# Optimization experiments

Hardware: AMD Instinct MI355X
Metric: run time of the kernel (lower is better)

The kernel has to match this reference:

```python
import jax, jax.numpy as jnp
import numpy as np

B, S, H = 2, 2048, 1024
NH = 16
HD = H // NH  # 64


def _linear_params(key, fan_in, fan_out):
    k1, k2 = jax.random.split(key)
    bound = 1.0 / np.sqrt(fan_in)
    W = jax.random.uniform(k1, (fan_in, fan_out), jnp.float32, -bound, bound)
    b = jax.random.uniform(k2, (fan_out,), jnp.float32, -bound, bound)
    return W, b


def setup_inputs() -> dict:
    key = jax.random.key(0)
    ks = jax.random.split(key, 7)
    hidden_states = jax.random.normal(ks[0], (B, S, H), jnp.float32)
    governance_embeddings = jax.random.normal(ks[1], (B, H), jnp.float32)
    Wq, bq = _linear_params(ks[2], H, H)
    Wk, bk = _linear_params(ks[3], H, H)
    Wv, bv = _linear_params(ks[4], H, H)
    Wgq, bgq = _linear_params(ks[5], H, H)
    Wgk, bgk = _linear_params(ks[6], H, H)
    return {
        'hidden_states': hidden_states,
        'governance_embeddings': governance_embeddings,
        'Wq': Wq, 'bq': bq, 'Wk': Wk, 'bk': bk, 'Wv': Wv, 'bv': bv,
        'Wgq': Wgq, 'bgq': bgq, 'Wgk': Wgk, 'bgk': bgk,
    }


def reference(hidden_states, governance_embeddings, Wq, bq, Wk, bk, Wv, bv, Wgq, bgq, Wgk, bgk):
    b, s, h = hidden_states.shape
    # QKV projections -> [b, nh, s, hd]
    def heads(x):
        return x.reshape(b, s, NH, HD).transpose(0, 2, 1, 3)
    q = heads(hidden_states @ Wq + bq)
    k = heads(hidden_states @ Wk + bk)
    v = heads(hidden_states @ Wv + bv)

    scale = jnp.float32(1.0 / np.sqrt(HD))
    scores = jnp.einsum('bhid,bhjd->bhij', q, k) * scale  # [b,nh,s,s]

    # governance bias: one query per example vs per-token keys (unscaled)
    gq = (governance_embeddings @ Wgq + bgq).reshape(b, NH, HD)      # [b,nh,hd]
    gk = (hidden_states @ Wgk + bgk).reshape(b, s, NH, HD)           # [b,s,nh,hd]
    gov_scores = jnp.einsum('bhd,bshd->bhs', gq, gk)                 # [b,nh,s]

    # bias is constant along key dim (torch expand on last axis)
    combined = scores + 0.1 * gov_scores[..., :, None]

    probs = jax.nn.softmax(combined, axis=-1)  # dropout = identity (eval)
    context = jnp.einsum('bhij,bhjd->bhid', probs, v)
    context = context.transpose(0, 2, 1, 3).reshape(b, s, h)

    entropy = -jnp.sum(probs * jnp.log(probs + 1e-8), axis=-1).mean()
    influence = jnp.abs(gov_scores).mean()  # mean over expanded tensor == mean over [b,nh,s]
    concentration = probs.max(axis=-1).mean()
    return context, entropy, influence, concentration
```

## Files before the change

kernel.cpp:

```cpp
#include <hip/hip_runtime.h>


typedef unsigned short u16;
typedef __attribute__((ext_vector_type(8))) short bf16x8;
typedef __attribute__((ext_vector_type(4))) float f32x4;
typedef __attribute__((ext_vector_type(4))) float float4v;

typedef const __attribute__((address_space(1))) void gvoid_t;
typedef __attribute__((address_space(3))) void lvoid_t;

__device__ __forceinline__ void gl_lds16(const void* g, void* l) {
  __builtin_amdgcn_global_load_lds((gvoid_t*)g, (lvoid_t*)l, 16, 0, 0);
}

__device__ __forceinline__ u16 f2bf(float x) {
  union { float f; unsigned u; } v; v.f = x;
  unsigned r = v.u + 0x7fffu + ((v.u >> 16) & 1u);
  return (u16)(r >> 16);
}
__device__ __forceinline__ float bf2f(u16 h) {
  union { unsigned u; float f; } v; v.u = ((unsigned)h) << 16; return v.f;
}
__device__ __forceinline__ unsigned pk2(float hi, float lo) {
  union { float f; unsigned u; } a, b; a.f = hi; b.f = lo;
  return __builtin_amdgcn_perm(a.u, b.u, 0x07060302u);
}

__global__ void prep(const float* __restrict__ hs,
                     const float* __restrict__ W0, const float* __restrict__ W1,
                     const float* __restrict__ W2, const float* __restrict__ W3,
                     const float* __restrict__ ge, const float* __restrict__ Wgq,
                     u16* __restrict__ hsB, u16* __restrict__ WB,
                     float* __restrict__ gq_part) {
  int bx = blockIdx.x, tid = threadIdx.x;
  if (bx < 2048) {
    int i = bx * 256 + tid;
    const float4v* in4 = (const float4v*)hs;
    float4v a = in4[i * 2], b = in4[i * 2 + 1];
    bf16x8 v;
    v[0] = (short)f2bf(a.x); v[1] = (short)f2bf(a.y);
    v[2] = (short)f2bf(a.z); v[3] = (short)f2bf(a.w);
    v[4] = (short)f2bf(b.x); v[5] = (short)f2bf(b.y);
    v[6] = (short)f2bf(b.z); v[7] = (short)f2bf(b.w);
    *(bf16x8*)&hsB[(size_t)i * 8] = v;
    return;
  }
  if (bx < 2560) {
    int idx = bx - 2048;
    int kb = idx & 127, mat = idx >> 7;
    const float* W = (mat == 0) ? W0 : (mat == 1) ? W1 : (mat == 2) ? W2 : W3;
    int n0 = tid * 4;
    float4v r[8];
#pragma unroll
    for (int j = 0; j < 8; ++j)
      r[j] = *(const float4v*)&W[(size_t)(kb * 8 + j) * 1024 + n0];
#pragma unroll
    for (int c = 0; c < 4; ++c) {
      uint4 o;
      o.x = pk2(r[1][c], r[0][c]); o.y = pk2(r[3][c], r[2][c]);
      o.z = pk2(r[5][c], r[4][c]); o.w = pk2(r[7][c], r[6][c]);
      *(uint4*)&WB[(size_t)(mat * 1024 + n0 + c) * 1024 + kb * 8] = o;
    }
    return;
  }
  {
    int idx = bx - 2560;
    int kb = idx >> 1, b = idx & 1;
    int col0 = tid * 4;
    float4v s = {0.f, 0.f, 0.f, 0.f};
    for (int k = kb * 32; k < kb * 32 + 32; ++k) {
      float g = ge[b * 1024 + k];
      float4v w = *(const float4v*)&Wgq[(size_t)k * 1024 + col0];
      s.x += g * w.x; s.y += g * w.y; s.z += g * w.z; s.w += g * w.w;
    }
    *(float4v*)&gq_part[(size_t)idx * 1024 + col0] = s;
  }
}

__global__ __launch_bounds__(256, 3) void gemm_qkvg(
    const u16* __restrict__ A, const u16* __restrict__ Bw,
    const float* __restrict__ bq, const float* __restrict__ bk,
    const float* __restrict__ bv, const float* __restrict__ bgk,
    const float* __restrict__ bgq, const float* __restrict__ gq_part,
    u16* __restrict__ Qb, u16* __restrict__ Kb,
    u16* __restrict__ GKb, u16* __restrict__ Vt,
    float* __restrict__ gq_final, float* __restrict__ acc3) {
  if (blockIdx.x == 1024) {
    int tid = threadIdx.x;
    if (tid < 3) acc3[tid] = 0.f;
#pragma unroll
    for (int i = 0; i < 8; ++i) {
      int t = tid + i * 256;
      float s = bgq[t & 1023];
      for (int kb = 0; kb < 32; ++kb) s += gq_part[(size_t)(kb * 2 + (t >> 10)) * 1024 + (t & 1023)];
      gq_final[t] = s;
    }
    return;
  }
  __shared__ __align__(16) u16 As[128 * 32];
  __shared__ __align__(16) u16 Bs[128 * 32];
  const int tid = threadIdx.x, lane = tid & 63, wv = tid >> 6;
  const int li = lane & 15, quad = lane >> 4;
  const int bid = blockIdx.x;
  const int nb = bid & 31, mb = bid >> 5;
  const u16* Ap = A + (size_t)(mb * 128) * 1024;
  const u16* Bp = Bw + (size_t)(nb * 128) * 1024;
  const int wm0 = (wv >> 1) * 64, wn0 = (wv & 1) * 64;

  f32x4 acc[4][4];
#pragma unroll
  for (int t = 0; t < 4; ++t)
#pragma unroll
    for (int u = 0; u < 4; ++u) acc[t][u] = (f32x4){0.f, 0.f, 0.f, 0.f};

  for (int kt = 0; kt < 32; ++kt) {
    __syncthreads();
#pragma unroll
    for (int jj = 0; jj < 2; ++jj) {
      int j = wv * 2 + jj;
      int row = j * 16 + (lane >> 2);
      int co = lane & 3;
      gl_lds16(Ap + (size_t)row * 1024 + kt * 32 + co * 8, &As[j * 512]);
      gl_lds16(Bp + (size_t)row * 1024 + kt * 32 + co * 8, &Bs[j * 512]);
    }
    __syncthreads();
    bf16x8 af[4], bf[4];
#pragma unroll
    for (int t = 0; t < 4; ++t)
      af[t] = *(const bf16x8*)&As[(wm0 + t * 16 + li) * 32 + quad * 8];
#pragma unroll
    for (int u = 0; u < 4; ++u)
      bf[u] = *(const bf16x8*)&Bs[(wn0 + u * 16 + li) * 32 + quad * 8];
#pragma unroll
    for (int t = 0; t < 4; ++t)
#pragma unroll
      for (int u = 0; u < 4; ++u)
        acc[t][u] = __builtin_amdgcn_mfma_f32_16x16x32_bf16(af[t], bf[u], acc[t][u], 0, 0, 0);
  }

  const int nbase = nb * 128;
  const int mat = nbase >> 10;
  if (mat == 2) {
#pragma unroll
    for (int t = 0; t < 4; ++t)
#pragma unroll
      for (int u = 0; u < 4; ++u) {
        int col = (nbase & 1023) + wn0 + u * 16 + li;
        float bb = bv[col];
        int row = mb * 128 + wm0 + t * 16 + quad * 4;
        int b = row >> 11, s = row & 2047;
        uint2 w;
        w.x = pk2(acc[t][u][1] + bb, acc[t][u][0] + bb);
        w.y = pk2(acc[t][u][3] + bb, acc[t][u][2] + bb);
        *(uint2*)&Vt[(size_t)b * (1024 * 2048) + (size_t)col * 2048 + s] = w;
      }
  } else {
    const float* bias = (mat == 0) ? bq : (mat == 1) ? bk : bgk;
    u16* outp = (mat == 0) ? Qb : (mat == 1) ? Kb : GKb;
    const float qscale = (mat == 0) ? 0.18033688f : 1.0f;
#pragma unroll
    for (int t = 0; t < 4; ++t)
#pragma unroll
      for (int u = 0; u < 4; ++u) {
        int col = (nbase & 1023) + wn0 + u * 16 + li;
        float bb = bias[col];
#pragma unroll
        for (int r = 0; r < 4; ++r) {
          int row = mb * 128 + wm0 + t * 16 + quad * 4 + r;
          outp[(size_t)row * 1024 + col] = f2bf((acc[t][u][r] + bb) * qscale);
        }
      }
  }
}

__global__ __launch_bounds__(256, 2) void attn_gov(
    const u16* __restrict__ Qb, const u16* __restrict__ Kb,
    const u16* __restrict__ Vt, const u16* __restrict__ GKb,
    const float* __restrict__ gq_final, float* __restrict__ out,
    float* __restrict__ acc3 ) {
  __shared__ __align__(16) u16 Ks[2][128 * 64];
  __shared__ __align__(16) u16 Vs[2][64 * 128];
  __shared__ __align__(16) u16 Ps[4][16 * 36];
  __shared__ float red[8];

  const int tid = threadIdx.x, lane = tid & 63, wv = tid >> 6;
  const int li = lane & 15, quad = lane >> 4;

  if (blockIdx.x >= 512) {
    int wid = (blockIdx.x - 512) * 4 + wv;
    int b = wid >> 11, s = wid & 2047;
    const u16* gk = GKb + (size_t)(b * 2048 + s) * 1024 + lane * 16;
    const float* gqp = gq_final + b * 1024 + lane * 16;
    bf16x8 g0 = *(const bf16x8*)gk, g1 = *(const bf16x8*)(gk + 8);
    float4v q0 = *(const float4v*)&gqp[0], q1 = *(const float4v*)&gqp[4];
    float4v q2 = *(const float4v*)&gqp[8], q3 = *(const float4v*)&gqp[12];
    float sum = 0.f;
    sum += bf2f((u16)g0[0]) * q0.x + bf2f((u16)g0[1]) * q0.y +
           bf2f((u16)g0[2]) * q0.z + bf2f((u16)g0[3]) * q0.w;
    sum += bf2f((u16)g0[4]) * q1.x + bf2f((u16)g0[5]) * q1.y +
           bf2f((u16)g0[6]) * q1.z + bf2f((u16)g0[7]) * q1.w;
    sum += bf2f((u16)g1[0]) * q2.x + bf2f((u16)g1[1]) * q2.y +
           bf2f((u16)g1[2]) * q2.z + bf2f((u16)g1[3]) * q2.w;
    sum += bf2f((u16)g1[4]) * q3.x + bf2f((u16)g1[5]) * q3.y +
           bf2f((u16)g1[6]) * q3.z + bf2f((u16)g1[7]) * q3.w;
    sum += __shfl_xor(sum, 1, 64);
    sum += __shfl_xor(sum, 2, 64);
    float v = ((lane & 3) == 0) ? fabsf(sum) : 0.f;
    v += __shfl_xor(v, 4, 64);  v += __shfl_xor(v, 8, 64);
    v += __shfl_xor(v, 16, 64); v += __shfl_xor(v, 32, 64);
    if (lane == 0) red[wv] = v;
    __syncthreads();
    if (tid == 0) atomicAdd(&acc3[2], red[0] + red[1] + red[2] + red[3]);
    return;
  }

  const int bx = blockIdx.x;
  const int bh = bx & 31, qb = bx >> 5;
  const int b = bh >> 4, h = bh & 15;
  const int wq0 = wv * 32;

  const u16* Qp = Qb + (size_t)(b * 2048 + qb * 128 + wq0) * 1024 + h * 64;
  const u16* Kp = Kb + (size_t)(b * 2048) * 1024 + h * 64;
  const u16* Vp = Vt + (size_t)b * (1024 * 2048) + (size_t)(h * 64) * 2048;

  bf16x8 qf[2][2];
#pragma unroll
  for (int t = 0; t < 2; ++t)
#pragma unroll
    for (int kc = 0; kc < 2; ++kc)
      qf[t][kc] = *(const bf16x8*)&Qp[(size_t)(t * 16 + li) * 1024 + kc * 32 + quad * 8];

  float m_st[2], l_st[2], e_st[2];
  f32x4 accO[4][2];
#pragma unroll
  for (int t = 0; t < 2; ++t) { m_st[t] = -3.0e38f; l_st[t] = 0.f; e_st[t] = 0.f; }
#pragma unroll
  for (int mt = 0; mt < 4; ++mt)
#pragma unroll
    for (int t = 0; t < 2; ++t) accO[mt][t] = (f32x4){0.f, 0.f, 0.f, 0.f};

#pragma unroll
  for (int jj = 0; jj < 4; ++jj) {
    int j = wv * 4 + jj;
    int row = j * 8 + (lane >> 3);
    int c16 = (lane & 7) ^ (row & 7);
    gl_lds16(Kp + (size_t)row * 1024 + c16 * 8, &Ks[0][j * 512]);
  }
#pragma unroll
  for (int jj = 0; jj < 4; ++jj) {
    int j = wv * 4 + jj;
    int row = j * 4 + (lane >> 4);
    int c16 = (lane & 15) ^ (row & 7);
    gl_lds16(Vp + (size_t)row * 2048 + c16 * 8, &Vs[0][j * 512]);
  }

  for (int kt = 0; kt < 16; ++kt) {
    const int cur = kt & 1;
    __syncthreads();
    if (kt < 15) {
      const u16* Kpt = Kp + (size_t)((kt + 1) * 128) * 1024;
#pragma unroll
      for (int jj = 0; jj < 4; ++jj) {
        int j = wv * 4 + jj;
        int row = j * 8 + (lane >> 3);
        int c16 = (lane & 7) ^ (row & 7);
        gl_lds16(Kpt + (size_t)row * 1024 + c16 * 8, &Ks[cur ^ 1][j * 512]);
      }
#pragma unroll
      for (int jj = 0; jj < 4; ++jj) {
        int j = wv * 4 + jj;
        int row = j * 4 + (lane >> 4);
        int c16 = (lane & 15) ^ (row & 7);
        gl_lds16(Vp + (size_t)row * 2048 + (kt + 1) * 128 + c16 * 8, &Vs[cur ^ 1][j * 512]);
      }
    }
    const u16* KsC = &Ks[cur][0];
    const u16* VsC = &Vs[cur][0];

    f32x4 S[8][2];
#pragma unroll
    for (int u = 0; u < 8; ++u) {
      int row = u * 16 + li;
      bf16x8 a0 = *(const bf16x8*)&KsC[row * 64 + ((quad) ^ (li & 7)) * 8];
      bf16x8 a1 = *(const bf16x8*)&KsC[row * 64 + ((4 + quad) ^ (li & 7)) * 8];
#pragma unroll
      for (int t = 0; t < 2; ++t) {
        f32x4 c = {0.f, 0.f, 0.f, 0.f};
        c = __builtin_amdgcn_mfma_f32_16x16x32_bf16(a0, qf[t][0], c, 0, 0, 0);
        c = __builtin_amdgcn_mfma_f32_16x16x32_bf16(a1, qf[t][1], c, 0, 0, 0);
        S[u][t] = c;
      }
    }

#pragma unroll
    for (int t = 0; t < 2; ++t) {
      float cmx = m_st[t], ps = 0.f, es = 0.f;
#pragma unroll
      for (int u = 0; u < 8; ++u)
#pragma unroll
        for (int r = 0; r < 4; ++r) {
          float s = S[u][t][r];
          cmx = fmaxf(cmx, s);
          float p = exp2f(s);
          ps += p;
          es = __builtin_fmaf(p, s, es);
          S[u][t][r] = p;
        }
      m_st[t] = cmx;
      l_st[t] += ps;
      e_st[t] += es;
    }

    u16* Pw = &Ps[wv][0];
#pragma unroll
    for (int c = 0; c < 4; ++c) {
      bf16x8 av[4];
#pragma unroll
      for (int mt = 0; mt < 4; ++mt) {
        int row = mt * 16 + li;
        av[mt] = *(const bf16x8*)&VsC[row * 128 + ((c * 4 + quad) ^ (li & 7)) * 8];
      }
#pragma unroll
      for (int t = 0; t < 2; ++t) {
        uint2 w0, w1;
        w0.x = pk2(S[2 * c][t][1], S[2 * c][t][0]);
        w0.y = pk2(S[2 * c][t][3], S[2 * c][t][2]);
        w1.x = pk2(S[2 * c + 1][t][1], S[2 * c + 1][t][0]);
        w1.y = pk2(S[2 * c + 1][t][3], S[2 * c + 1][t][2]);
        *(uint2*)&Pw[li * 36 + quad * 4] = w0;
        *(uint2*)&Pw[li * 36 + 16 + quad * 4] = w1;
        bf16x8 bp = *(const bf16x8*)&Pw[li * 36 + quad * 8];
#pragma unroll
        for (int mt = 0; mt < 4; ++mt)
          accO[mt][t] = __builtin_amdgcn_mfma_f32_16x16x32_bf16(av[mt], bp, accO[mt][t], 0, 0, 0);
      }
    }
  }

  float* outp = out + (size_t)(b * 2048 + qb * 128 + wq0) * 1024 + h * 64;
  float entw = 0.f, concw = 0.f;
#pragma unroll
  for (int t = 0; t < 2; ++t) {
    float lsum = l_st[t];
    lsum += __shfl_xor(lsum, 16, 64); lsum += __shfl_xor(lsum, 32, 64);
    float esum = e_st[t];
    esum += __shfl_xor(esum, 16, 64); esum += __shfl_xor(esum, 32, 64);
    float mm = m_st[t];
    mm = fmaxf(mm, __shfl_xor(mm, 16, 64)); mm = fmaxf(mm, __shfl_xor(mm, 32, 64));
    float inv = 1.0f / lsum;
    entw += __logf(lsum) - 0.69314718f * esum * inv;
    concw += exp2f(mm) * inv;
#pragma unroll
    for (int mt = 0; mt < 4; ++mt) {
      f32x4 o = accO[mt][t];
      o[0] *= inv; o[1] *= inv; o[2] *= inv; o[3] *= inv;
      *(float4v*)&outp[(size_t)(t * 16 + li) * 1024 + mt * 16 + quad * 4] = *(float4v*)&o;
    }
  }
#pragma unroll
  for (int off = 1; off < 64; off <<= 1) {
    entw += __shfl_xor(entw, off, 64);
    concw += __shfl_xor(concw, off, 64);
  }
  if (lane == 0) { red[wv] = entw * 0.25f; red[4 + wv] = concw * 0.25f; }
  __syncthreads();
  if (tid == 0) {
    atomicAdd(&acc3[0], red[0] + red[1] + red[2] + red[3]);
    atomicAdd(&acc3[1], red[4] + red[5] + red[6] + red[7]);
  }
}

__global__ void finalize(const float* __restrict__ acc3, float* __restrict__ out) {
  if (threadIdx.x == 0) {
    out[0] = acc3[0] * (1.f / 65536.f);
    out[1] = acc3[2] * (1.f / 65536.f);
    out[2] = acc3[1] * (1.f / 65536.f);
  }
}

extern "C" void kernel_launch(void* const* d_in, const int* in_sizes, int n_in,
                              void* d_out, int out_size, void* d_ws, size_t ws_size,
                              hipStream_t stream) {
  (void)in_sizes; (void)n_in; (void)out_size; (void)ws_size;
  const float* hs  = (const float*)d_in[0];
  const float* ge  = (const float*)d_in[1];
  const float* Wq  = (const float*)d_in[2];
  const float* bq  = (const float*)d_in[3];
  const float* Wk  = (const float*)d_in[4];
  const float* bk  = (const float*)d_in[5];
  const float* Wv  = (const float*)d_in[6];
  const float* bv  = (const float*)d_in[7];
  const float* Wgq = (const float*)d_in[8];
  const float* bgq = (const float*)d_in[9];
  const float* Wgk = (const float*)d_in[10];
  const float* bgk = (const float*)d_in[11];

  char* ws = (char*)d_ws;
  u16* hsB = (u16*)(ws);
  u16* WB  = (u16*)(ws + (size_t)(8 << 20));
  u16* Qb  = (u16*)(ws + (size_t)(16 << 20));
  u16* Kb  = (u16*)(ws + (size_t)(24 << 20));
  u16* Vt  = (u16*)(ws + (size_t)(32 << 20));
  u16* GKb = (u16*)(ws + (size_t)(40 << 20));
  float* gq_part  = (float*)(ws + (size_t)(48 << 20));
  float* gq_final = (float*)(ws + (size_t)(48 << 20) + 262144);
  float* acc3     = (float*)(ws + (size_t)(48 << 20) + 524288);
  float* out = (float*)d_out;

  prep<<<2624, 256, 0, stream>>>(hs, Wq, Wk, Wv, Wgk, ge, Wgq, hsB, WB, gq_part);
  gemm_qkvg<<<1025, 256, 0, stream>>>(hsB, WB, bq, bk, bv, bgk, bgq, gq_part,
                                      Qb, Kb, GKb, Vt, gq_final, acc3);
  attn_gov<<<1536, 256, 0, stream>>>(Qb, Kb, Vt, GKb, gq_final, out, acc3);
  finalize<<<1, 64, 0, stream>>>(acc3, out + 4194304);
}
```

Before: 254.9 us.

## Use 32x32 MFMA with permlane P reshuffle in attention; split gov kernel; tiled weight transpose

The attention inner loop moves from 16x16x32 MFMA tiles to 32x32x16 tiles, one query row per lane pair. The P tile is reshaped in registers with permlane32_swap (ds_bpermute as a fallback) instead of a round trip through shared memory. The governance-score reduction becomes its own kernel instead of extra blocks in the attention launch. The weight conversion in prep now goes through a shared-memory tiled transpose with coalesced reads and writes. Together these aim to cut LDS traffic and instruction count in attention and make the weight conversion coalesced, at the cost of an extra launch and higher register pressure from the 16-float accumulators.

```diff
diff --git a/kernel.cpp b/kernel.cpp
--- a/kernel.cpp
+++ b/kernel.cpp
@@ -4,7 +4,10 @@
 typedef unsigned short u16;
 typedef __attribute__((ext_vector_type(8))) short bf16x8;
 typedef __attribute__((ext_vector_type(4))) float f32x4;
+typedef __attribute__((ext_vector_type(16))) float f32x16;
+typedef __attribute__((ext_vector_type(4))) u16 u16x4;
 typedef __attribute__((ext_vector_type(4))) float float4v;
+typedef __attribute__((ext_vector_type(2))) unsigned uint2v;
 
 typedef const __attribute__((address_space(1))) void gvoid_t;
 typedef __attribute__((address_space(3))) void lvoid_t;
@@ -24,6 +27,29 @@
 __device__ __forceinline__ unsigned pk2(float hi, float lo) {
   union { float f; unsigned u; } a, b; a.f = hi; b.f = lo;
   return __builtin_amdgcn_perm(a.u, b.u, 0x07060302u);
+}
+__device__ __forceinline__ bf16x8 mk8(unsigned a, unsigned b, unsigned c, unsigned d) {
+  union { unsigned u[4]; bf16x8 v; } x;
+  x.u[0] = a; x.u[1] = b; x.u[2] = c; x.u[3] = d; return x.v;
+}
+
+#if defined(__has_builtin)
+#if __has_builtin(__builtin_amdgcn_permlane32_swap)
+#define HAVE_PLSWAP 1
+#endif
+#endif
+
+__device__ __forceinline__ void plswap(unsigned& a, unsigned& b, int lane) {
+#ifdef HAVE_PLSWAP
+  uint2v r = __builtin_amdgcn_permlane32_swap(a, b, false, false);
+  a = r.x; b = r.y;
+#else
+  unsigned ca = __builtin_amdgcn_ds_bpermute((lane ^ 32) << 2, a);
+  unsigned cb = __builtin_amdgcn_ds_bpermute((lane ^ 32) << 2, b);
+  unsigned na = (lane < 32) ? a : cb;
+  unsigned nb = (lane < 32) ? ca : b;
+  a = na; b = nb;
+#endif
 }
 
 __global__ void prep(const float* __restrict__ hs,
@@ -32,6 +58,7 @@
                      const float* __restrict__ ge, const float* __restrict__ Wgq,
                      u16* __restrict__ hsB, u16* __restrict__ WB,
                      float* __restrict__ gq_part) {
+  __shared__ __align__(16) u16 T[64][72];
   int bx = blockIdx.x, tid = threadIdx.x;
   if (bx < 2048) {
     int i = bx * 256 + tid;
@@ -45,26 +72,33 @@
     *(bf16x8*)&hsB[(size_t)i * 8] = v;
     return;
   }
-  if (bx < 2560) {
+  if (bx < 3072) {
     int idx = bx - 2048;
-    int kb = idx & 127, mat = idx >> 7;
+    int mat = idx >> 8, sub = idx & 255;
     const float* W = (mat == 0) ? W0 : (mat == 1) ? W1 : (mat == 2) ? W2 : W3;
-    int n0 = tid * 4;
-    float4v r[8];
-#pragma unroll
-    for (int j = 0; j < 8; ++j)
-      r[j] = *(const float4v*)&W[(size_t)(kb * 8 + j) * 1024 + n0];
-#pragma unroll
-    for (int c = 0; c < 4; ++c) {
-      uint4 o;
-      o.x = pk2(r[1][c], r[0][c]); o.y = pk2(r[3][c], r[2][c]);
-      o.z = pk2(r[5][c], r[4][c]); o.w = pk2(r[7][c], r[6][c]);
-      *(uint4*)&WB[(size_t)(mat * 1024 + n0 + c) * 1024 + kb * 8] = o;
+    int k0 = (sub >> 4) * 64, n0 = (sub & 15) * 64;
+#pragma unroll
+    for (int p = 0; p < 4; ++p) {
+      int chunk = p * 256 + tid;
+      int row = chunk >> 4, cp = chunk & 15;
+      float4v v = *(const float4v*)&W[(size_t)(k0 + row) * 1024 + n0 + cp * 4];
+      u16x4 o; o.x = f2bf(v.x); o.y = f2bf(v.y); o.z = f2bf(v.z); o.w = f2bf(v.w);
+      *(u16x4*)&T[row][cp * 4] = o;
+    }
+    __syncthreads();
+#pragma unroll
+    for (int p = 0; p < 2; ++p) {
+      int chunk = p * 256 + tid;
+      int nrow = chunk >> 3, cp = chunk & 7;
+      bf16x8 v;
+#pragma unroll
+      for (int e = 0; e < 8; ++e) v[e] = (short)T[cp * 8 + e][nrow];
+      *(bf16x8*)&WB[(size_t)(mat * 1024 + n0 + nrow) * 1024 + k0 + cp * 8] = v;
     }
     return;
   }
   {
-    int idx = bx - 2560;
+    int idx = bx - 3072;
     int kb = idx >> 1, b = idx & 1;
     int col0 = tid * 4;
     float4v s = {0.f, 0.f, 0.f, 0.f};
@@ -92,7 +126,8 @@
     for (int i = 0; i < 8; ++i) {
       int t = tid + i * 256;
       float s = bgq[t & 1023];
-      for (int kb = 0; kb < 32; ++kb) s += gq_part[(size_t)(kb * 2 + (t >> 10)) * 1024 + (t & 1023)];
+      for (int kb = 0; kb < 32; ++kb)
+        s += gq_part[(size_t)(kb * 2 + (t >> 10)) * 1024 + (t & 1023)];
       gq_final[t] = s;
     }
     return;
@@ -173,71 +208,35 @@
   }
 }
 
-__global__ __launch_bounds__(256, 2) void attn_gov(
+__global__ __launch_bounds__(256, 2) void attn_kernel(
     const u16* __restrict__ Qb, const u16* __restrict__ Kb,
-    const u16* __restrict__ Vt, const u16* __restrict__ GKb,
-    const float* __restrict__ gq_final, float* __restrict__ out,
+    const u16* __restrict__ Vt, float* __restrict__ out,
     float* __restrict__ acc3 ) {
   __shared__ __align__(16) u16 Ks[2][128 * 64];
   __shared__ __align__(16) u16 Vs[2][64 * 128];
-  __shared__ __align__(16) u16 Ps[4][16 * 36];
   __shared__ float red[8];
 
   const int tid = threadIdx.x, lane = tid & 63, wv = tid >> 6;
-  const int li = lane & 15, quad = lane >> 4;
-
-  if (blockIdx.x >= 512) {
-    int wid = (blockIdx.x - 512) * 4 + wv;
-    int b = wid >> 11, s = wid & 2047;
-    const u16* gk = GKb + (size_t)(b * 2048 + s) * 1024 + lane * 16;
-    const float* gqp = gq_final + b * 1024 + lane * 16;
-    bf16x8 g0 = *(const bf16x8*)gk, g1 = *(const bf16x8*)(gk + 8);
-    float4v q0 = *(const float4v*)&gqp[0], q1 = *(const float4v*)&gqp[4];
-    float4v q2 = *(const float4v*)&gqp[8], q3 = *(const float4v*)&gqp[12];
-    float sum = 0.f;
-    sum += bf2f((u16)g0[0]) * q0.x + bf2f((u16)g0[1]) * q0.y +
-           bf2f((u16)g0[2]) * q0.z + bf2f((u16)g0[3]) * q0.w;
-    sum += bf2f((u16)g0[4]) * q1.x + bf2f((u16)g0[5]) * q1.y +
-           bf2f((u16)g0[6]) * q1.z + bf2f((u16)g0[7]) * q1.w;
-    sum += bf2f((u16)g1[0]) * q2.x + bf2f((u16)g1[1]) * q2.y +
-           bf2f((u16)g1[2]) * q2.z + bf2f((u16)g1[3]) * q2.w;
-    sum += bf2f((u16)g1[4]) * q3.x + bf2f((u16)g1[5]) * q3.y +
-           bf2f((u16)g1[6]) * q3.z + bf2f((u16)g1[7]) * q3.w;
-    sum += __shfl_xor(sum, 1, 64);
-    sum += __shfl_xor(sum, 2, 64);
-    float v = ((lane & 3) == 0) ? fabsf(sum) : 0.f;
-    v += __shfl_xor(v, 4, 64);  v += __shfl_xor(v, 8, 64);
-    v += __shfl_xor(v, 16, 64); v += __shfl_xor(v, 32, 64);
-    if (lane == 0) red[wv] = v;
-    __syncthreads();
-    if (tid == 0) atomicAdd(&acc3[2], red[0] + red[1] + red[2] + red[3]);
-    return;
-  }
-
+  const int q_l = lane & 31, half = lane >> 5;
   const int bx = blockIdx.x;
   const int bh = bx & 31, qb = bx >> 5;
   const int b = bh >> 4, h = bh & 15;
-  const int wq0 = wv * 32;
-
-  const u16* Qp = Qb + (size_t)(b * 2048 + qb * 128 + wq0) * 1024 + h * 64;
+
+  const u16* Qp = Qb + (size_t)(b * 2048 + qb * 128 + wv * 32 + q_l) * 1024 + h * 64;
   const u16* Kp = Kb + (size_t)(b * 2048) * 1024 + h * 64;
   const u16* Vp = Vt + (size_t)b * (1024 * 2048) + (size_t)(h * 64) * 2048;
 
-  bf16x8 qf[2][2];
-#pragma unroll
-  for (int t = 0; t < 2; ++t)
-#pragma unroll
-    for (int kc = 0; kc < 2; ++kc)
-      qf[t][kc] = *(const bf16x8*)&Qp[(size_t)(t * 16 + li) * 1024 + kc * 32 + quad * 8];
-
-  float m_st[2], l_st[2], e_st[2];
-  f32x4 accO[4][2];
-#pragma unroll
-  for (int t = 0; t < 2; ++t) { m_st[t] = -3.0e38f; l_st[t] = 0.f; e_st[t] = 0.f; }
-#pragma unroll
-  for (int mt = 0; mt < 4; ++mt)
-#pragma unroll
-    for (int t = 0; t < 2; ++t) accO[mt][t] = (f32x4){0.f, 0.f, 0.f, 0.f};
+  bf16x8 qf[4];
+#pragma unroll
+  for (int s = 0; s < 4; ++s)
+    qf[s] = *(const bf16x8*)&Qp[s * 16 + half * 8];
+
+  float m_st = -3.0e38f, l_st = 0.f, e_st = 0.f;
+  f32x16 accO[2];
+#pragma unroll
+  for (int dt = 0; dt < 2; ++dt)
+#pragma unroll
+    for (int r = 0; r < 16; ++r) accO[dt][r] = 0.f;
 
 #pragma unroll
   for (int jj = 0; jj < 4; ++jj) {
@@ -277,97 +276,111 @@
     const u16* KsC = &Ks[cur][0];
     const u16* VsC = &Vs[cur][0];
 
-    f32x4 S[8][2];
-#pragma unroll
-    for (int u = 0; u < 8; ++u) {
-      int row = u * 16 + li;
-      bf16x8 a0 = *(const bf16x8*)&KsC[row * 64 + ((quad) ^ (li & 7)) * 8];
-      bf16x8 a1 = *(const bf16x8*)&KsC[row * 64 + ((4 + quad) ^ (li & 7)) * 8];
-#pragma unroll
-      for (int t = 0; t < 2; ++t) {
-        f32x4 c = {0.f, 0.f, 0.f, 0.f};
-        c = __builtin_amdgcn_mfma_f32_16x16x32_bf16(a0, qf[t][0], c, 0, 0, 0);
-        c = __builtin_amdgcn_mfma_f32_16x16x32_bf16(a1, qf[t][1], c, 0, 0, 0);
-        S[u][t] = c;
-      }
-    }
-
-#pragma unroll
-    for (int t = 0; t < 2; ++t) {
-      float cmx = m_st[t], ps = 0.f, es = 0.f;
-#pragma unroll
-      for (int u = 0; u < 8; ++u)
-#pragma unroll
-        for (int r = 0; r < 4; ++r) {
-          float s = S[u][t][r];
-          cmx = fmaxf(cmx, s);
-          float p = exp2f(s);
-          ps += p;
-          es = __builtin_fmaf(p, s, es);
-          S[u][t][r] = p;
-        }
-      m_st[t] = cmx;
-      l_st[t] += ps;
-      e_st[t] += es;
-    }
-
-    u16* Pw = &Ps[wv][0];
-#pragma unroll
-    for (int c = 0; c < 4; ++c) {
-      bf16x8 av[4];
-#pragma unroll
-      for (int mt = 0; mt < 4; ++mt) {
-        int row = mt * 16 + li;
-        av[mt] = *(const bf16x8*)&VsC[row * 128 + ((c * 4 + quad) ^ (li & 7)) * 8];
-      }
-#pragma unroll
-      for (int t = 0; t < 2; ++t) {
-        uint2 w0, w1;
-        w0.x = pk2(S[2 * c][t][1], S[2 * c][t][0]);
-        w0.y = pk2(S[2 * c][t][3], S[2 * c][t][2]);
-        w1.x = pk2(S[2 * c + 1][t][1], S[2 * c + 1][t][0]);
-        w1.y = pk2(S[2 * c + 1][t][3], S[2 * c + 1][t][2]);
-        *(uint2*)&Pw[li * 36 + quad * 4] = w0;
-        *(uint2*)&Pw[li * 36 + 16 + quad * 4] = w1;
-        bf16x8 bp = *(const bf16x8*)&Pw[li * 36 + quad * 8];
-#pragma unroll
-        for (int mt = 0; mt < 4; ++mt)
-          accO[mt][t] = __builtin_amdgcn_mfma_f32_16x16x32_bf16(av[mt], bp, accO[mt][t], 0, 0, 0);
-      }
-    }
-  }
-
-  float* outp = out + (size_t)(b * 2048 + qb * 128 + wq0) * 1024 + h * 64;
-  float entw = 0.f, concw = 0.f;
-#pragma unroll
-  for (int t = 0; t < 2; ++t) {
-    float lsum = l_st[t];
-    lsum += __shfl_xor(lsum, 16, 64); lsum += __shfl_xor(lsum, 32, 64);
-    float esum = e_st[t];
-    esum += __shfl_xor(esum, 16, 64); esum += __shfl_xor(esum, 32, 64);
-    float mm = m_st[t];
-    mm = fmaxf(mm, __shfl_xor(mm, 16, 64)); mm = fmaxf(mm, __shfl_xor(mm, 32, 64));
-    float inv = 1.0f / lsum;
-    entw += __logf(lsum) - 0.69314718f * esum * inv;
-    concw += exp2f(mm) * inv;
-#pragma unroll
-    for (int mt = 0; mt < 4; ++mt) {
-      f32x4 o = accO[mt][t];
-      o[0] *= inv; o[1] *= inv; o[2] *= inv; o[3] *= inv;
-      *(float4v*)&outp[(size_t)(t * 16 + li) * 1024 + mt * 16 + quad * 4] = *(float4v*)&o;
-    }
-  }
+    float ps = 0.f, es = 0.f, cmx = m_st;
+#pragma unroll
+    for (int u = 0; u < 4; ++u) {
+      f32x16 c;
+#pragma unroll
+      for (int r = 0; r < 16; ++r) c[r] = 0.f;
+#pragma unroll
+      for (int s = 0; s < 4; ++s) {
+        int p = (2 * s + half) ^ (q_l & 7);
+        bf16x8 a = *(const bf16x8*)&KsC[(u * 32 + q_l) * 64 + p * 8];
+        c = __builtin_amdgcn_mfma_f32_32x32x16_bf16(a, qf[s], c, 0, 0, 0);
+      }
+#pragma unroll
+      for (int r = 0; r < 16; ++r) {
+        float sv = c[r];
+        cmx = fmaxf(cmx, sv);
+        float pe = exp2f(sv);
+        ps += pe;
+        es = __builtin_fmaf(pe, sv, es);
+        c[r] = pe;
+      }
+      unsigned p0 = pk2(c[1], c[0]),  p1 = pk2(c[3], c[2]);
+      unsigned p2 = pk2(c[5], c[4]),  p3 = pk2(c[7], c[6]);
+      unsigned p4 = pk2(c[9], c[8]),  p5 = pk2(c[11], c[10]);
+      unsigned p6 = pk2(c[13], c[12]), p7 = pk2(c[15], c[14]);
+      plswap(p0, p2, lane); plswap(p1, p3, lane);
+      plswap(p4, p6, lane); plswap(p5, p7, lane);
+      bf16x8 bf0 = mk8(p0, p1, p2, p3);
+      bf16x8 bf1 = mk8(p4, p5, p6, p7);
+#pragma unroll
+      for (int dt = 0; dt < 2; ++dt) {
+        int d = dt * 32 + q_l;
+        int pa = (u * 4 + half) ^ (d & 7);
+        int pb = (u * 4 + 2 + half) ^ (d & 7);
+        bf16x8 av0 = *(const bf16x8*)&VsC[d * 128 + pa * 8];
+        accO[dt] = __builtin_amdgcn_mfma_f32_32x32x16_bf16(av0, bf0, accO[dt], 0, 0, 0);
+        bf16x8 av1 = *(const bf16x8*)&VsC[d * 128 + pb * 8];
+        accO[dt] = __builtin_amdgcn_mfma_f32_32x32x16_bf16(av1, bf1, accO[dt], 0, 0, 0);
+      }
+    }
+    m_st = cmx;
+    l_st += ps;
+    e_st += es;
+  }
+
+  float lsum = l_st + __shfl_xor(l_st, 32, 64);
+  float esum = e_st + __shfl_xor(e_st, 32, 64);
+  float mm = fmaxf(m_st, __shfl_xor(m_st, 32, 64));
+  float inv = 1.0f / lsum;
+  float entw = __logf(lsum) - 0.69314718f * esum * inv;
+  float concw = exp2f(mm) * inv;
+
+  float* outp = out + (size_t)(b * 2048 + qb * 128 + wv * 32 + q_l) * 1024 + h * 64;
+#pragma unroll
+  for (int dt = 0; dt < 2; ++dt)
+#pragma unroll
+    for (int g = 0; g < 4; ++g) {
+      float4v o;
+      o.x = accO[dt][4 * g + 0] * inv; o.y = accO[dt][4 * g + 1] * inv;
+      o.z = accO[dt][4 * g + 2] * inv; o.w = accO[dt][4 * g + 3] * inv;
+      *(float4v*)&outp[dt * 32 + 8 * g + 4 * half] = o;
+    }
+
 #pragma unroll
   for (int off = 1; off < 64; off <<= 1) {
     entw += __shfl_xor(entw, off, 64);
     concw += __shfl_xor(concw, off, 64);
   }
-  if (lane == 0) { red[wv] = entw * 0.25f; red[4 + wv] = concw * 0.25f; }
+  if (lane == 0) { red[wv] = entw * 0.5f; red[4 + wv] = concw * 0.5f; }
   __syncthreads();
   if (tid == 0) {
     atomicAdd(&acc3[0], red[0] + red[1] + red[2] + red[3]);
     atomicAdd(&acc3[1], red[4] + red[5] + red[6] + red[7]);
   }
+}
+
+__global__ void gov_kernel(const u16* __restrict__ GKb, const float* __restrict__ gq,
+                           float* __restrict__ acc_inf) {
+  __shared__ float redI[4];
+  int lane = threadIdx.x & 63, wv = threadIdx.x >> 6;
+  int wid = blockIdx.x * 4 + wv;
+  int b = wid >> 11, s = wid & 2047;
+  const u16* gk = GKb + (size_t)(b * 2048 + s) * 1024 + lane * 16;
+  const float* gqp = gq + b * 1024 + lane * 16;
+  bf16x8 g0 = *(const bf16x8*)gk, g1 = *(const bf16x8*)(gk + 8);
+  float4v q0 = *(const float4v*)&gqp[0], q1 = *(const float4v*)&gqp[4];
+  float4v q2 = *(const float4v*)&gqp[8], q3 = *(const float4v*)&gqp[12];
+  float sum = 0.f;
+  sum += bf2f((u16)g0[0]) * q0.x + bf2f((u16)g0[1]) * q0.y +
+         bf2f((u16)g0[2]) * q0.z + bf2f((u16)g0[3]) * q0.w;
+  sum += bf2f((u16)g0[4]) * q1.x + bf2f((u16)g0[5]) * q1.y +
+         bf2f((u16)g0[6]) * q1.z + bf2f((u16)g0[7]) * q1.w;
+  sum += bf2f((u16)g1[0]) * q2.x + bf2f((u16)g1[1]) * q2.y +
+         bf2f((u16)g1[2]) * q2.z + bf2f((u16)g1[3]) * q2.w;
+  sum += bf2f((u16)g1[4]) * q3.x + bf2f((u16)g1[5]) * q3.y +
+         bf2f((u16)g1[6]) * q3.z + bf2f((u16)g1[7]) * q3.w;
+  sum += __shfl_xor(sum, 1, 64);
+  sum += __shfl_xor(sum, 2, 64);
+  float v = ((lane & 3) == 0) ? fabsf(sum) : 0.f;
+  v += __shfl_xor(v, 4, 64);  v += __shfl_xor(v, 8, 64);
+  v += __shfl_xor(v, 16, 64); v += __shfl_xor(v, 32, 64);
+  if (lane == 0) redI[wv] = v;
+  __syncthreads();
+  if (threadIdx.x == 0)
+    atomicAdd(acc_inf, redI[0] + redI[1] + redI[2] + redI[3]);
 }
 
 __global__ void finalize(const float* __restrict__ acc3, float* __restrict__ out) {
@@ -407,9 +420,10 @@
   float* acc3     = (float*)(ws + (size_t)(48 << 20) + 524288);
   float* out = (float*)d_out;
 
-  prep<<<2624, 256, 0, stream>>>(hs, Wq, Wk, Wv, Wgk, ge, Wgq, hsB, WB, gq_part);
+  prep<<<3136, 256, 0, stream>>>(hs, Wq, Wk, Wv, Wgk, ge, Wgq, hsB, WB, gq_part);
   gemm_qkvg<<<1025, 256, 0, stream>>>(hsB, WB, bq, bk, bv, bgk, bgq, gq_part,
                                       Qb, Kb, GKb, Vt, gq_final, acc3);
-  attn_gov<<<1536, 256, 0, stream>>>(Qb, Kb, Vt, GKb, gq_final, out, acc3);
+  attn_kernel<<<512, 256, 0, stream>>>(Qb, Kb, Vt, out, acc3);
+  gov_kernel<<<1024, 256, 0, stream>>>(GKb, gq_final, acc3 + 2);
   finalize<<<1, 64, 0, stream>>>(acc3, out + 4194304);
 }
```

After: 232.3 us. -8.9%, faster.
